# Optimization experiments

Measured on AMD Instinct MI355X. Metric: run time of the kernel, lower is better.

The kernel has to match this reference:

```python
import jax, jax.numpy as jnp
import numpy as np

H = 50  # hidden_size

def setup_inputs() -> dict:
    key = jax.random.key(0)
    ks = jax.random.split(key, 7)
    B, T, I = 8192, 2048, 1
    s_ih = 1.0 / np.sqrt(H)
    x = jax.random.normal(ks[0], (B, T, I), dtype=jnp.float32)
    # PyTorch nn.LSTM params, gate order (i, f, g, o)
    W_ih = jax.random.uniform(ks[1], (4 * H, I), minval=-s_ih, maxval=s_ih, dtype=jnp.float32)
    W_hh = jax.random.uniform(ks[2], (4 * H, H), minval=-s_ih, maxval=s_ih, dtype=jnp.float32)
    b_ih = jax.random.uniform(ks[3], (4 * H,), minval=-s_ih, maxval=s_ih, dtype=jnp.float32)
    b_hh = jax.random.uniform(ks[4], (4 * H,), minval=-s_ih, maxval=s_ih, dtype=jnp.float32)
    W_lin = jax.random.uniform(ks[5], (1, H), minval=-s_ih, maxval=s_ih, dtype=jnp.float32)
    b_lin = jax.random.uniform(ks[6], (1,), minval=-s_ih, maxval=s_ih, dtype=jnp.float32)
    return {"x": x, "W_ih": W_ih, "W_hh": W_hh, "b_ih": b_ih, "b_hh": b_hh,
            "W_lin": W_lin, "b_lin": b_lin}

def _lstm_last_h(x, W_ih, W_hh, b_ih, b_hh):
    B = x.shape[0]
    # precompute input contribution per timestep: [T, B, 4H]
    xg = jnp.einsum('bti,gi->tbg', x, W_ih) + (b_ih + b_hh)  # [T,B,4H]

    def step(carry, xg_t):
        h, c = carry
        z = xg_t + h @ W_hh.T  # [B,4H]
        i = jax.nn.sigmoid(z[:, :H])
        f = jax.nn.sigmoid(z[:, H:2 * H])
        g = jnp.tanh(z[:, 2 * H:3 * H])
        o = jax.nn.sigmoid(z[:, 3 * H:])
        c = f * c + i * g
        h = o * jnp.tanh(c)
        return (h, c), None

    h0 = jnp.zeros((B, H), dtype=x.dtype)
    c0 = jnp.zeros((B, H), dtype=x.dtype)
    (h_last, _), _ = jax.lax.scan(step, (h0, c0), xg)
    return h_last  # [B,H]

def reference(x, W_ih, W_hh, b_ih, b_hh, W_lin, b_lin):
    h_last = _lstm_last_h(x, W_ih, W_hh, b_ih, b_hh)
    return h_last @ W_lin.T + b_lin  # [B,1]
```

## Files before the change

### kernel.cpp

```cpp
#include <hip/hip_runtime.h>


#define HID   50
#define NSTEP 2048
#define BPB   16
#define HSTR  72

typedef _Float16 half8   __attribute__((ext_vector_type(8)));
typedef float    float4v __attribute__((ext_vector_type(4)));

__device__ __forceinline__ float gate_pair(float zi, float zf, float zg, float zo,
                                           float& c) {
    float ei = __builtin_amdgcn_exp2f(zi);
    float ef = __builtin_amdgcn_exp2f(zf);
    float Eg = __builtin_amdgcn_exp2f(zg);
    float eo = __builtin_amdgcn_exp2f(zo);
    float t1  = (1.0f + ei) * (1.0f + Eg);
    float num = c * t1 + (1.0f + ef) * (Eg - 1.0f);
    float D   = t1 * (1.0f + ef);
    c = num * __builtin_amdgcn_rcpf(D);
    float a  = fminf(fmaxf(2.8853900817779268f * c, -24.0f), 24.0f);
    float Ec = __builtin_amdgcn_exp2f(a);
    return (Ec - 1.0f) * __builtin_amdgcn_rcpf((1.0f + eo) * (1.0f + Ec));
}

__global__ __launch_bounds__(256, 2) void lstm_fused(
    const float* __restrict__ x,
    const float* __restrict__ W_ih,
    const float* __restrict__ W_hh,
    const float* __restrict__ b_ih,
    const float* __restrict__ b_hh,
    const float* __restrict__ W_lin,
    const float* __restrict__ b_lin,
    float* __restrict__ out)
{
    __shared__ __align__(16) _Float16 hbuf[2][BPB][HSTR];

    const int tid  = threadIdx.x;
    const int wave = tid >> 6;
    const int lane = tid & 63;
    const int col  = lane & 15;
    const int quad = lane >> 4;
    const int b0   = blockIdx.x * BPB;
    const int j    = wave * 16 + col;

    for (int i = tid; i < 2 * BPB * HSTR; i += 256)
        (&hbuf[0][0][0])[i] = (_Float16)0.0f;
    __syncthreads();
    if (tid < BPB) {
        hbuf[0][tid][HID]     = (_Float16)x[(size_t)(b0 + tid) * NSTEP];
        hbuf[0][tid][HID + 1] = (_Float16)1.0f;
        hbuf[1][tid][HID + 1] = (_Float16)1.0f;
    }

    const float LOG2E = 1.4426950408889634f;
    half8 bfrag[4][2];
    for (int g = 0; g < 4; ++g) {
        const float sc = (g == 2) ? (2.0f * LOG2E) : (-LOG2E);
        for (int kt = 0; kt < 2; ++kt) {
            half8 f;
            #pragma unroll
            for (int jj = 0; jj < 8; ++jj) {
                int k = kt * 32 + quad * 8 + jj;
                float v = 0.0f;
                if (j < HID) {
                    int row = g * HID + j;
                    if (k < HID)           v = W_hh[row * HID + k];
                    else if (k == HID)     v = W_ih[row];
                    else if (k == HID + 1) v = b_ih[row] + b_hh[row];
                }
                f[jj] = (_Float16)(v * sc);
            }
            bfrag[g][kt] = f;
        }
    }

    float c[4] = {0.f, 0.f, 0.f, 0.f};
    const bool xloader = (wave == 3) && (quad == 0);
    const float* xrow = x + (size_t)(b0 + col) * NSTEP;
    const float4v Z4 = {0.f, 0.f, 0.f, 0.f};

    __syncthreads();

#define STEP(CUR, NXT, T)                                                        \
    {                                                                            \
        float xn = 0.f;                                                          \
        if (xloader) {                                                           \
            int tt = ((T) + 1 < NSTEP) ? ((T) + 1) : (NSTEP - 1);                \
            xn = xrow[tt];                                                       \
        }                                                                        \
        const _Float16* arow = &hbuf[CUR][col][0];                               \
        half8 a0 = *(const half8*)(arow + quad * 8);                             \
        half8 a1 = *(const half8*)(arow + 32 + quad * 8);                        \
        float4v d0, d1, d2, d3;                                                  \
        d0 = __builtin_amdgcn_mfma_f32_16x16x32_f16(a0, bfrag[0][0], Z4, 0, 0, 0); \
        d1 = __builtin_amdgcn_mfma_f32_16x16x32_f16(a0, bfrag[1][0], Z4, 0, 0, 0); \
        d2 = __builtin_amdgcn_mfma_f32_16x16x32_f16(a0, bfrag[2][0], Z4, 0, 0, 0); \
        d3 = __builtin_amdgcn_mfma_f32_16x16x32_f16(a0, bfrag[3][0], Z4, 0, 0, 0); \
        d0 = __builtin_amdgcn_mfma_f32_16x16x32_f16(a1, bfrag[0][1], d0, 0, 0, 0); \
        d1 = __builtin_amdgcn_mfma_f32_16x16x32_f16(a1, bfrag[1][1], d1, 0, 0, 0); \
        d2 = __builtin_amdgcn_mfma_f32_16x16x32_f16(a1, bfrag[2][1], d2, 0, 0, 0); \
        d3 = __builtin_amdgcn_mfma_f32_16x16x32_f16(a1, bfrag[3][1], d3, 0, 0, 0); \
        _Float16 hv[4];                                                          \
        _Pragma("unroll")                                                        \
        for (int r = 0; r < 4; ++r)                                              \
            hv[r] = (_Float16)gate_pair(d0[r], d1[r], d2[r], d3[r], c[r]);       \
        if (j < HID) {                                                           \
            _Pragma("unroll")                                                    \
            for (int r = 0; r < 4; ++r)                                          \
                hbuf[NXT][quad * 4 + r][j] = hv[r];                              \
        }                                                                        \
        if (xloader)                                                             \
            hbuf[NXT][col][HID] = (_Float16)xn;                                  \
        __syncthreads();                                                         \
    }

    for (int t = 0; t < NSTEP; t += 2) {
        STEP(0, 1, t)
        STEP(1, 0, t + 1)
    }
#undef STEP

    if (tid < BPB) {
        float s = b_lin[0];
        for (int k = 0; k < HID; ++k)
            s += (float)hbuf[0][tid][k] * W_lin[k];
        out[b0 + tid] = s;
    }
}

extern "C" void kernel_launch(void* const* d_in, const int* in_sizes, int n_in,
                              void* d_out, int out_size, void* d_ws, size_t ws_size,
                              hipStream_t stream) {
    const float* x     = (const float*)d_in[0];
    const float* W_ih  = (const float*)d_in[1];
    const float* W_hh  = (const float*)d_in[2];
    const float* b_ih  = (const float*)d_in[3];
    const float* b_hh  = (const float*)d_in[4];
    const float* W_lin = (const float*)d_in[5];
    const float* b_lin = (const float*)d_in[6];
    float* outp = (float*)d_out;
    dim3 grid(8192 / BPB), block(256);
    hipLaunchKernelGGL(lstm_fused, grid, block, 0, stream,
                       x, W_ih, W_hh, b_ih, b_hh, W_lin, b_lin, outp);
}
```

Baseline: 1.366 ms.

## Process two 16-row batch groups per block to interleave independent MFMA chains

Each block now handles 32 batch rows as two independent 16-row groups, and each wave issues two interleaved MFMA chains and gate computations per step. The aim is instruction-level parallelism inside a wave, hiding MFMA and transcendental latency in the serial recurrence, and halving the number of barriers per batch row. In exchange the grid is half as large, launch bounds drop to one block per SIMD group, and register pressure rises, which may reduce occupancy.

```diff
diff --git a/kernel.cpp b/kernel.cpp
--- a/kernel.cpp
+++ b/kernel.cpp
@@ -3,7 +3,8 @@
 
 #define HID   50
 #define NSTEP 2048
-#define BPB   16
+#define GPB   2
+#define BPB   32
 #define HSTR  72
 
 typedef _Float16 half8   __attribute__((ext_vector_type(8)));
@@ -24,7 +25,7 @@
     return (Ec - 1.0f) * __builtin_amdgcn_rcpf((1.0f + eo) * (1.0f + Ec));
 }
 
-__global__ __launch_bounds__(256, 2) void lstm_fused(
+__global__ __launch_bounds__(256, 1) void lstm_fused(
     const float* __restrict__ x,
     const float* __restrict__ W_ih,
     const float* __restrict__ W_hh,
@@ -34,7 +35,7 @@
     const float* __restrict__ b_lin,
     float* __restrict__ out)
 {
-    __shared__ __align__(16) _Float16 hbuf[2][BPB][HSTR];
+    __shared__ __align__(16) _Float16 hbuf[GPB][2][16][HSTR];
 
     const int tid  = threadIdx.x;
     const int wave = tid >> 6;
@@ -44,13 +45,14 @@
     const int b0   = blockIdx.x * BPB;
     const int j    = wave * 16 + col;
 
-    for (int i = tid; i < 2 * BPB * HSTR; i += 256)
-        (&hbuf[0][0][0])[i] = (_Float16)0.0f;
+    for (int i = tid; i < GPB * 2 * 16 * HSTR; i += 256)
+        (&hbuf[0][0][0][0])[i] = (_Float16)0.0f;
     __syncthreads();
     if (tid < BPB) {
-        hbuf[0][tid][HID]     = (_Float16)x[(size_t)(b0 + tid) * NSTEP];
-        hbuf[0][tid][HID + 1] = (_Float16)1.0f;
-        hbuf[1][tid][HID + 1] = (_Float16)1.0f;
+        int g = tid >> 4, r = tid & 15;
+        hbuf[g][0][r][HID]     = (_Float16)x[(size_t)(b0 + tid) * NSTEP];
+        hbuf[g][0][r][HID + 1] = (_Float16)1.0f;
+        hbuf[g][1][r][HID + 1] = (_Float16)1.0f;
     }
 
     const float LOG2E = 1.4426950408889634f;
@@ -75,43 +77,52 @@
         }
     }
 
-    float c[4] = {0.f, 0.f, 0.f, 0.f};
-    const bool xloader = (wave == 3) && (quad == 0);
-    const float* xrow = x + (size_t)(b0 + col) * NSTEP;
+    float c0[4] = {0.f, 0.f, 0.f, 0.f};
+    float c1[4] = {0.f, 0.f, 0.f, 0.f};
+    const bool xl = (wave < GPB) && (quad == 0);
+    const float* xrow = x + (size_t)(b0 + wave * 16 + col) * NSTEP;
     const float4v Z4 = {0.f, 0.f, 0.f, 0.f};
 
     __syncthreads();
 
+#define MFMA16(A, B, C) __builtin_amdgcn_mfma_f32_16x16x32_f16(A, B, C, 0, 0, 0)
 #define STEP(CUR, NXT, T)                                                        \
     {                                                                            \
         float xn = 0.f;                                                          \
-        if (xloader) {                                                           \
+        if (xl) {                                                                \
             int tt = ((T) + 1 < NSTEP) ? ((T) + 1) : (NSTEP - 1);                \
             xn = xrow[tt];                                                       \
         }                                                                        \
-        const _Float16* arow = &hbuf[CUR][col][0];                               \
-        half8 a0 = *(const half8*)(arow + quad * 8);                             \
-        half8 a1 = *(const half8*)(arow + 32 + quad * 8);                        \
-        float4v d0, d1, d2, d3;                                                  \
-        d0 = __builtin_amdgcn_mfma_f32_16x16x32_f16(a0, bfrag[0][0], Z4, 0, 0, 0); \
-        d1 = __builtin_amdgcn_mfma_f32_16x16x32_f16(a0, bfrag[1][0], Z4, 0, 0, 0); \
-        d2 = __builtin_amdgcn_mfma_f32_16x16x32_f16(a0, bfrag[2][0], Z4, 0, 0, 0); \
-        d3 = __builtin_amdgcn_mfma_f32_16x16x32_f16(a0, bfrag[3][0], Z4, 0, 0, 0); \
-        d0 = __builtin_amdgcn_mfma_f32_16x16x32_f16(a1, bfrag[0][1], d0, 0, 0, 0); \
-        d1 = __builtin_amdgcn_mfma_f32_16x16x32_f16(a1, bfrag[1][1], d1, 0, 0, 0); \
-        d2 = __builtin_amdgcn_mfma_f32_16x16x32_f16(a1, bfrag[2][1], d2, 0, 0, 0); \
-        d3 = __builtin_amdgcn_mfma_f32_16x16x32_f16(a1, bfrag[3][1], d3, 0, 0, 0); \
-        _Float16 hv[4];                                                          \
+        const _Float16* ar0 = &hbuf[0][CUR][col][0];                             \
+        const _Float16* ar1 = &hbuf[1][CUR][col][0];                             \
+        half8 a00 = *(const half8*)(ar0 + quad * 8);                             \
+        half8 a10 = *(const half8*)(ar1 + quad * 8);                             \
+        half8 a01 = *(const half8*)(ar0 + 32 + quad * 8);                        \
+        half8 a11 = *(const half8*)(ar1 + 32 + quad * 8);                        \
+        float4v e0, e1, e2, e3, f0, f1, f2, f3;                                  \
+        e0 = MFMA16(a00, bfrag[0][0], Z4);  f0 = MFMA16(a10, bfrag[0][0], Z4);   \
+        e1 = MFMA16(a00, bfrag[1][0], Z4);  f1 = MFMA16(a10, bfrag[1][0], Z4);   \
+        e2 = MFMA16(a00, bfrag[2][0], Z4);  f2 = MFMA16(a10, bfrag[2][0], Z4);   \
+        e3 = MFMA16(a00, bfrag[3][0], Z4);  f3 = MFMA16(a10, bfrag[3][0], Z4);   \
+        e0 = MFMA16(a01, bfrag[0][1], e0);  f0 = MFMA16(a11, bfrag[0][1], f0);   \
+        e1 = MFMA16(a01, bfrag[1][1], e1);  f1 = MFMA16(a11, bfrag[1][1], f1);   \
+        e2 = MFMA16(a01, bfrag[2][1], e2);  f2 = MFMA16(a11, bfrag[2][1], f2);   \
+        e3 = MFMA16(a01, bfrag[3][1], e3);  f3 = MFMA16(a11, bfrag[3][1], f3);   \
+        _Float16 hv0[4], hv1[4];                                                 \
         _Pragma("unroll")                                                        \
-        for (int r = 0; r < 4; ++r)                                              \
-            hv[r] = (_Float16)gate_pair(d0[r], d1[r], d2[r], d3[r], c[r]);       \
+        for (int r = 0; r < 4; ++r) {                                            \
+            hv0[r] = (_Float16)gate_pair(e0[r], e1[r], e2[r], e3[r], c0[r]);     \
+            hv1[r] = (_Float16)gate_pair(f0[r], f1[r], f2[r], f3[r], c1[r]);     \
+        }                                                                        \
         if (j < HID) {                                                           \
             _Pragma("unroll")                                                    \
-            for (int r = 0; r < 4; ++r)                                          \
-                hbuf[NXT][quad * 4 + r][j] = hv[r];                              \
+            for (int r = 0; r < 4; ++r) {                                        \
+                hbuf[0][NXT][quad * 4 + r][j] = hv0[r];                          \
+                hbuf[1][NXT][quad * 4 + r][j] = hv1[r];                          \
+            }                                                                    \
         }                                                                        \
-        if (xloader)                                                             \
-            hbuf[NXT][col][HID] = (_Float16)xn;                                  \
+        if (xl)                                                                  \
+            hbuf[wave][NXT][col][HID] = (_Float16)xn;                            \
         __syncthreads();                                                         \
     }
 
@@ -120,11 +131,13 @@
         STEP(1, 0, t + 1)
     }
 #undef STEP
+#undef MFMA16
 
     if (tid < BPB) {
+        int g = tid >> 4, r = tid & 15;
         float s = b_lin[0];
         for (int k = 0; k < HID; ++k)
-            s += (float)hbuf[0][tid][k] * W_lin[k];
+            s += (float)hbuf[g][0][r][k] * W_lin[k];
         out[b0 + tid] = s;
     }
 }
```

After: 1.593 ms. 16.6% more time.

## Halve batch rows per block and spread rows to even MFMA tile rows

Applied to the files above, without the earlier changes.

Each block now handles 8 batch rows instead of 16. The rows sit at even positions of the 16-row MFMA tile, so each lane evaluates only two gate nonlinearities per step instead of four. Launch bounds rise to 4 blocks per CU and the grid doubles, giving more resident waves to hide the serial per-step latency. In exchange, half of every MFMA's rows do no useful work and there are twice as many blocks, each paying barriers and weight-fragment setup.

```diff
diff --git a/kernel.cpp b/kernel.cpp
--- a/kernel.cpp
+++ b/kernel.cpp
@@ -3,7 +3,7 @@
 
 #define HID   50
 #define NSTEP 2048
-#define BPB   16
+#define BPB   8
 #define HSTR  72
 
 typedef _Float16 half8   __attribute__((ext_vector_type(8)));
@@ -24,7 +24,7 @@
     return (Ec - 1.0f) * __builtin_amdgcn_rcpf((1.0f + eo) * (1.0f + Ec));
 }
 
-__global__ __launch_bounds__(256, 2) void lstm_fused(
+__global__ __launch_bounds__(256, 4) void lstm_fused(
     const float* __restrict__ x,
     const float* __restrict__ W_ih,
     const float* __restrict__ W_hh,
@@ -34,7 +34,7 @@
     const float* __restrict__ b_lin,
     float* __restrict__ out)
 {
-    __shared__ __align__(16) _Float16 hbuf[2][BPB][HSTR];
+    __shared__ __align__(16) _Float16 hbuf[2][16][HSTR];
 
     const int tid  = threadIdx.x;
     const int wave = tid >> 6;
@@ -44,13 +44,13 @@
     const int b0   = blockIdx.x * BPB;
     const int j    = wave * 16 + col;
 
-    for (int i = tid; i < 2 * BPB * HSTR; i += 256)
+    for (int i = tid; i < 2 * 16 * HSTR; i += 256)
         (&hbuf[0][0][0])[i] = (_Float16)0.0f;
     __syncthreads();
     if (tid < BPB) {
-        hbuf[0][tid][HID]     = (_Float16)x[(size_t)(b0 + tid) * NSTEP];
-        hbuf[0][tid][HID + 1] = (_Float16)1.0f;
-        hbuf[1][tid][HID + 1] = (_Float16)1.0f;
+        hbuf[0][2 * tid][HID]     = (_Float16)x[(size_t)(b0 + tid) * NSTEP];
+        hbuf[0][2 * tid][HID + 1] = (_Float16)1.0f;
+        hbuf[1][2 * tid][HID + 1] = (_Float16)1.0f;
     }
 
     const float LOG2E = 1.4426950408889634f;
@@ -75,17 +75,18 @@
         }
     }
 
-    float c[4] = {0.f, 0.f, 0.f, 0.f};
-    const bool xloader = (wave == 3) && (quad == 0);
+    float c0 = 0.f, c1 = 0.f;
+    const bool xl = (wave == 3) && (quad == 0) && (col < BPB);
     const float* xrow = x + (size_t)(b0 + col) * NSTEP;
     const float4v Z4 = {0.f, 0.f, 0.f, 0.f};
 
     __syncthreads();
 
+#define MFMA16(A, B, C) __builtin_amdgcn_mfma_f32_16x16x32_f16(A, B, C, 0, 0, 0)
 #define STEP(CUR, NXT, T)                                                        \
     {                                                                            \
         float xn = 0.f;                                                          \
-        if (xloader) {                                                           \
+        if (xl) {                                                                \
             int tt = ((T) + 1 < NSTEP) ? ((T) + 1) : (NSTEP - 1);                \
             xn = xrow[tt];                                                       \
         }                                                                        \
@@ -93,25 +94,23 @@
         half8 a0 = *(const half8*)(arow + quad * 8);                             \
         half8 a1 = *(const half8*)(arow + 32 + quad * 8);                        \
         float4v d0, d1, d2, d3;                                                  \
-        d0 = __builtin_amdgcn_mfma_f32_16x16x32_f16(a0, bfrag[0][0], Z4, 0, 0, 0); \
-        d1 = __builtin_amdgcn_mfma_f32_16x16x32_f16(a0, bfrag[1][0], Z4, 0, 0, 0); \
-        d2 = __builtin_amdgcn_mfma_f32_16x16x32_f16(a0, bfrag[2][0], Z4, 0, 0, 0); \
-        d3 = __builtin_amdgcn_mfma_f32_16x16x32_f16(a0, bfrag[3][0], Z4, 0, 0, 0); \
-        d0 = __builtin_amdgcn_mfma_f32_16x16x32_f16(a1, bfrag[0][1], d0, 0, 0, 0); \
-        d1 = __builtin_amdgcn_mfma_f32_16x16x32_f16(a1, bfrag[1][1], d1, 0, 0, 0); \
-        d2 = __builtin_amdgcn_mfma_f32_16x16x32_f16(a1, bfrag[2][1], d2, 0, 0, 0); \
-        d3 = __builtin_amdgcn_mfma_f32_16x16x32_f16(a1, bfrag[3][1], d3, 0, 0, 0); \
-        _Float16 hv[4];                                                          \
-        _Pragma("unroll")                                                        \
-        for (int r = 0; r < 4; ++r)                                              \
-            hv[r] = (_Float16)gate_pair(d0[r], d1[r], d2[r], d3[r], c[r]);       \
+        d0 = MFMA16(a0, bfrag[0][0], Z4);                                        \
+        d1 = MFMA16(a0, bfrag[1][0], Z4);                                        \
+        d2 = MFMA16(a0, bfrag[2][0], Z4);                                        \
+        d3 = MFMA16(a0, bfrag[3][0], Z4);                                        \
+        d0 = MFMA16(a1, bfrag[0][1], d0);                                        \
+        d1 = MFMA16(a1, bfrag[1][1], d1);                                        \
+        d2 = MFMA16(a1, bfrag[2][1], d2);                                        \
+        d3 = MFMA16(a1, bfrag[3][1], d3);                                        \
+            \
+        _Float16 h0 = (_Float16)gate_pair(d0[0], d1[0], d2[0], d3[0], c0);       \
+        _Float16 h1 = (_Float16)gate_pair(d0[2], d1[2], d2[2], d3[2], c1);       \
         if (j < HID) {                                                           \
-            _Pragma("unroll")                                                    \
-            for (int r = 0; r < 4; ++r)                                          \
-                hbuf[NXT][quad * 4 + r][j] = hv[r];                              \
+            hbuf[NXT][quad * 4][j]     = h0;                                     \
+            hbuf[NXT][quad * 4 + 2][j] = h1;                                     \
         }                                                                        \
-        if (xloader)                                                             \
-            hbuf[NXT][col][HID] = (_Float16)xn;                                  \
+        if (xl)                                                                  \
+            hbuf[NXT][2 * col][HID] = (_Float16)xn;                              \
         __syncthreads();                                                         \
     }
 
@@ -120,11 +119,12 @@
         STEP(1, 0, t + 1)
     }
 #undef STEP
+#undef MFMA16
 
     if (tid < BPB) {
         float s = b_lin[0];
         for (int k = 0; k < HID; ++k)
-            s += (float)hbuf[0][tid][k] * W_lin[k];
+            s += (float)hbuf[0][2 * tid][k] * W_lin[k];
         out[b0 + tid] = s;
     }
 }
```

Result: slower. 1.426 ms (+4.4%).
